# Optimization experiments

Measured on AMD Instinct MI355X. Metric: run time of the kernel, lower is better.

Reference implementation:

```python
import jax, jax.numpy as jnp
import numpy as np

N_NODES = 2048
N_ELEMS = 4096

# kind codes
KIND_R, KIND_IVS, KIND_VC, KIND_SW = 0, 1, 2, 3


def setup_inputs() -> dict:
    key = jax.random.key(0)
    k1, k2, k3 = jax.random.split(key, 3)
    M = jax.random.normal(k1, (N_NODES, N_ELEMS), dtype=jnp.float32)
    params = jax.random.uniform(k2, (N_ELEMS,), dtype=jnp.float32)
    kinds = jax.random.randint(k3, (N_ELEMS,), 0, 4, dtype=jnp.int32)
    return {"M": M, "params": params, "kinds": kinds}


def reference(M, params, kinds):
    N, E = M.shape
    W = 2 * E + N  # column width of every row block
    dt = M.dtype

    # kcl rows: [M | 0_{N,E} | 0_{N,N}]
    kcl = jnp.concatenate([M, jnp.zeros((N, E + N), dtype=dt)], axis=1)
    # kvl rows: [0_{E,E} | I_E | -M^T]
    kvl = jnp.concatenate(
        [jnp.zeros((E, E), dtype=dt), jnp.eye(E, dtype=dt), -M.T], axis=1
    )

    is_r = kinds == KIND_R
    is_ivs = kinds == KIND_IVS
    is_vc = kinds == KIND_VC
    is_sw = kinds == KIND_SW
    sw_on = params > 0

    one = jnp.ones((), dtype=dt)
    zero = jnp.zeros((), dtype=dt)
    # z-column value at pos: R -> -param, VC -> 1, SW(off) -> 1, else 0
    z_val = jnp.where(is_r, -params,
             jnp.where(is_vc | (is_sw & ~sw_on), one, zero)).astype(dt)
    # y-column value at E+pos: R -> 1, IVS -> 1, SW(on) -> 1, else 0
    y_val = jnp.where(is_r | is_ivs | (is_sw & sw_on), one, zero).astype(dt)

    pos = jnp.arange(E)
    elem = jnp.zeros((E, W), dtype=dt)
    elem = elem.at[pos, pos].set(z_val)
    elem = elem.at[pos, E + pos].set(y_val)

    return jnp.concatenate([kcl, kvl, elem], axis=0)
```

## Files before the change

### kernel.cpp

```cpp
#include <hip/hip_runtime.h>

#define NN 2048
#define EE 4096
#define WW 10240
#define TOT_ROWS 10240

typedef float v4f __attribute__((ext_vector_type(4)));

#define TP_BLOCKS 512

__device__ __forceinline__ void nt_store(float* p, v4f v) {
    __builtin_nontemporal_store(v, (v4f*)p);
}

__global__ __launch_bounds__(256) void coeff_kernel(
    const float* __restrict__ M,
    const float* __restrict__ params,
    const int*   __restrict__ kinds,
    float*       __restrict__ out)
{
    int tid = threadIdx.x;

    if (blockIdx.x < TP_BLOCKS) {
        __shared__ __align__(16) float t[4][64 * 64];
        int cT = (blockIdx.x & 63) << 6;
        int rT = (blockIdx.x >> 6) << 8;
        int r = tid & 15, q = tid >> 4;
        int c0 = r * 4;

        #pragma unroll
        for (int w = 0; w < 4; ++w) {
            #pragma unroll
            for (int it = 0; it < 4; ++it) {
                int lrow = it * 16 + q;
                int grow = rT + w * 64 + lrow;
                v4f val = *(const v4f*)(M + (size_t)grow * EE + cT + c0);
                nt_store(out + (size_t)grow * WW + cT + c0, val);
                #pragma unroll
                for (int s = 0; s < 4; ++s) {
                    int i = (s + (r >> 2)) & 3;
                    int c = c0 + i;
                    t[w][c * 64 + (lrow ^ ((c & 15) * 4))] = val[i];
                }
            }
        }
        __syncthreads();

        #pragma unroll
        for (int it = 0; it < 4; ++it) {
            int e  = it * 16 + q;
            int j0 = r * 4;
            float* dst = out + (size_t)(NN + cT + e) * WW + 2 * EE + rT + j0;
            #pragma unroll
            for (int w = 0; w < 4; ++w) {
                v4f v = *(const v4f*)(&t[w][e * 64 + (j0 ^ ((e & 15) * 4))]);
                v4f nv = { -v[0], -v[1], -v[2], -v[3] };
                nt_store(dst + w * 64, nv);
            }
        }
    } else {
        int row = blockIdx.x - TP_BLOCKS;
        int tid4 = tid * 4;
        float* dst = out + (size_t)row * WW;
        const v4f zero = {0.f, 0.f, 0.f, 0.f};

        if (row < NN) {
            #pragma unroll
            for (int k = 4; k < 10; ++k)
                nt_store(dst + k * 1024 + tid4, zero);
        } else if (row < NN + EE) {
            int e = row - NN;
            int col_y = EE + e;
            #pragma unroll
            for (int k = 0; k < 8; ++k) {
                int base = k * 1024 + tid4;
                v4f v = zero;
                #pragma unroll
                for (int j = 0; j < 4; ++j)
                    if (base + j == col_y) v[j] = 1.0f;
                nt_store(dst + base, v);
            }
        } else {
            int e = row - (NN + EE);
            float p = params[e];
            int kk = kinds[e];
            bool on = p > 0.0f;
            float z, y;
            if (kk == 0)      { z = -p;             y = 1.0f; }
            else if (kk == 1) { z = 0.0f;           y = 1.0f; }
            else if (kk == 2) { z = 1.0f;           y = 0.0f; }
            else              { z = on ? 0.f : 1.f; y = on ? 1.f : 0.f; }
            int col_z = e, col_y = EE + e;
            #pragma unroll
            for (int k = 0; k < 10; ++k) {
                int base = k * 1024 + tid4;
                v4f v = zero;
                #pragma unroll
                for (int j = 0; j < 4; ++j) {
                    if (base + j == col_z) v[j] = z;
                    if (base + j == col_y) v[j] = y;
                }
                nt_store(dst + base, v);
            }
        }
    }
}

extern "C" void kernel_launch(void* const* d_in, const int* in_sizes, int n_in,
                              void* d_out, int out_size, void* d_ws, size_t ws_size,
                              hipStream_t stream) {
    const float* M      = (const float*)d_in[0];
    const float* params = (const float*)d_in[1];
    const int*   kinds  = (const int*)d_in[2];
    float*       out    = (float*)d_out;

    coeff_kernel<<<TP_BLOCKS + TOT_ROWS, 256, 0, stream>>>(M, params, kinds, out);
}
```

Before: 429.2 us.

## Move M copy into row blocks and retile transpose to 32x512 tiles

The direct copy of M into the kcl rows moves out of the transpose blocks and into the row-fill blocks, so each of those blocks writes its full 10240-wide row. The transpose blocks now come after the row blocks in launch order. They use 32-column by 512-row tiles, so each output row segment written is 2KB of contiguous data instead of 256B pieces. The transpose no longer stores the copied tile, and the swizzle pattern changes. The costs are that M is read twice, once by the row blocks and once by the transpose blocks, and the new tile's XOR swizzle may cause LDS bank conflicts.

```diff
diff --git a/kernel.cpp b/kernel.cpp
--- a/kernel.cpp
+++ b/kernel.cpp
@@ -21,50 +21,19 @@
 {
     int tid = threadIdx.x;
 
-    if (blockIdx.x < TP_BLOCKS) {
-        __shared__ __align__(16) float t[4][64 * 64];
-        int cT = (blockIdx.x & 63) << 6;
-        int rT = (blockIdx.x >> 6) << 8;
-        int r = tid & 15, q = tid >> 4;
-        int c0 = r * 4;
-
-        #pragma unroll
-        for (int w = 0; w < 4; ++w) {
-            #pragma unroll
-            for (int it = 0; it < 4; ++it) {
-                int lrow = it * 16 + q;
-                int grow = rT + w * 64 + lrow;
-                v4f val = *(const v4f*)(M + (size_t)grow * EE + cT + c0);
-                nt_store(out + (size_t)grow * WW + cT + c0, val);
-                #pragma unroll
-                for (int s = 0; s < 4; ++s) {
-                    int i = (s + (r >> 2)) & 3;
-                    int c = c0 + i;
-                    t[w][c * 64 + (lrow ^ ((c & 15) * 4))] = val[i];
-                }
-            }
-        }
-        __syncthreads();
-
-        #pragma unroll
-        for (int it = 0; it < 4; ++it) {
-            int e  = it * 16 + q;
-            int j0 = r * 4;
-            float* dst = out + (size_t)(NN + cT + e) * WW + 2 * EE + rT + j0;
-            #pragma unroll
-            for (int w = 0; w < 4; ++w) {
-                v4f v = *(const v4f*)(&t[w][e * 64 + (j0 ^ ((e & 15) * 4))]);
-                v4f nv = { -v[0], -v[1], -v[2], -v[3] };
-                nt_store(dst + w * 64, nv);
-            }
-        }
-    } else {
-        int row = blockIdx.x - TP_BLOCKS;
+    if (blockIdx.x < TOT_ROWS) {
+        int row = blockIdx.x;
         int tid4 = tid * 4;
         float* dst = out + (size_t)row * WW;
         const v4f zero = {0.f, 0.f, 0.f, 0.f};
 
         if (row < NN) {
+            const float* src = M + (size_t)row * EE;
+            #pragma unroll
+            for (int k = 0; k < 4; ++k) {
+                int off = k * 1024 + tid4;
+                nt_store(dst + off, *(const v4f*)(src + off));
+            }
             #pragma unroll
             for (int k = 4; k < 10; ++k)
                 nt_store(dst + k * 1024 + tid4, zero);
@@ -103,6 +72,33 @@
                 nt_store(dst + base, v);
             }
         }
+    } else {
+        __shared__ __align__(16) float t[32 * 512];
+        int tpIdx = blockIdx.x - TOT_ROWS;
+        int cT = (tpIdx & 127) << 5;
+        int rT = (tpIdx >> 7) << 9;
+
+        #pragma unroll
+        for (int pass = 0; pass < 16; ++pass) {
+            int rr = pass * 32 + (tid >> 3);
+            int c0 = (tid & 7) * 4;
+            v4f val = *(const v4f*)(M + (size_t)(rT + rr) * EE + cT + c0);
+            #pragma unroll
+            for (int i = 0; i < 4; ++i) {
+                int c = c0 + i;
+                t[c * 512 + (rr ^ (c & 28))] = val[i];
+            }
+        }
+        __syncthreads();
+
+        #pragma unroll
+        for (int pass = 0; pass < 16; ++pass) {
+            int e   = pass * 2 + (tid >> 7);
+            int rr0 = (tid & 127) * 4;
+            v4f v = *(const v4f*)(&t[e * 512 + (rr0 ^ (e & 28))]);
+            v4f nv = { -v[0], -v[1], -v[2], -v[3] };
+            nt_store(out + (size_t)(NN + cT + e) * WW + 2 * EE + rT + rr0, nv);
+        }
     }
 }
 
@@ -114,5 +110,5 @@
     const int*   kinds  = (const int*)d_in[2];
     float*       out    = (float*)d_out;
 
-    coeff_kernel<<<TP_BLOCKS + TOT_ROWS, 256, 0, stream>>>(M, params, kinds, out);
+    coeff_kernel<<<TOT_ROWS + TP_BLOCKS, 256, 0, stream>>>(M, params, kinds, out);
 }
```

Result: no change. 426.1 us (median of 2 runs) (-0.7%).
